# Kernel tuning notes

Measured on AMD Instinct MI355X. Metric: run time of the kernel, lower is better.

The kernel has to match this reference:

```python
import jax, jax.numpy as jnp
import numpy as np

P0 = 2   # tublet_size
P = 16   # patch_size
FC = 2   # flow channels (map_x, map_y)


def patchify(x, p0, p1, p2):
    # x: (B, C, T, H, W) -> (B, (T/p0)(H/p1)(W/p2), p0*p1*p2*C)
    B, C, T, H, W = x.shape
    x = x.reshape(B, C, T // p0, p0, H // p1, p1, W // p2, p2)
    x = x.transpose(0, 2, 4, 6, 3, 5, 7, 1)  # b t h w p0 p1 p2 c
    return x.reshape(B, (T // p0) * (H // p1) * (W // p2), p0 * p1 * p2 * C)


def unpatchify(x, p0, p1, p2, C, T, H, W):
    # x: (B, N, p0*p1*p2*C) -> (B, C, T, H, W)
    B = x.shape[0]
    x = x.reshape(B, T // p0, H // p1, W // p2, p0, p1, p2, C)
    x = x.transpose(0, 7, 1, 4, 2, 5, 3, 6)  # b c t p0 h p1 w p2
    return x.reshape(B, C, T, H, W)


def bilinear_warp(imgs, mx, my):
    # imgs: (B, C, T, H, W); mx, my: (B, T, H, W) absolute sample coords.
    # Equivalent of cv2.remap INTER_LINEAR with constant (zero) border.
    B, C, T, H, W = imgs.shape
    x0 = jnp.floor(mx)
    y0 = jnp.floor(my)
    wx = (mx - x0).reshape(B, 1, T, H * W)
    wy = (my - y0).reshape(B, 1, T, H * W)
    x0i = x0.astype(jnp.int32)
    y0i = y0.astype(jnp.int32)
    imgs_flat = imgs.reshape(B, C, T, H * W)

    def gather(yi, xi):
        yc = jnp.clip(yi, 0, H - 1)
        xc = jnp.clip(xi, 0, W - 1)
        idx = (yc * W + xc).reshape(B, 1, T, H * W)
        v = jnp.take_along_axis(imgs_flat, jnp.broadcast_to(idx, (B, C, T, H * W)), axis=-1)
        valid = ((yi >= 0) & (yi <= H - 1) & (xi >= 0) & (xi <= W - 1)).reshape(B, 1, T, H * W)
        return v * valid.astype(v.dtype)

    v00 = gather(y0i, x0i)
    v01 = gather(y0i, x0i + 1)
    v10 = gather(y0i + 1, x0i)
    v11 = gather(y0i + 1, x0i + 1)
    out = (v00 * (1 - wx) * (1 - wy) + v01 * wx * (1 - wy)
           + v10 * (1 - wx) * wy + v11 * wx * wy)
    return out.reshape(B, C, T, H, W)


def setup_inputs() -> dict:
    key = jax.random.key(0)
    k1, k2, k3 = jax.random.split(key, 3)
    B, C, T, H, W = 8, 3, 16, 224, 224
    N = (T // P0) * (H // P) * (W // P)         # 1568 tokens
    D = P0 * P * P * FC                         # 1024 per-token flow dim
    output = jax.random.normal(k1, (B, N, D), dtype=jnp.float32)
    raw_target = jax.random.normal(k2, (B, C, T, H, W), dtype=jnp.float32)
    mask = jax.random.randint(k3, (B, N), 0, 2) > 0
    return {"output": output, "raw_target": raw_target, "mask": mask}


def reference(output, raw_target, mask):
    B, C, T, H, W = raw_target.shape
    # tokens -> dense flow field (B, 2, T, H, W)
    flows = unpatchify(output, P0, P, P, FC, T, H, W)
    gx = jnp.arange(W, dtype=flows.dtype)               # (W,)
    gy = jnp.arange(H, dtype=flows.dtype)[:, None]      # (H, 1)
    mx = flows[:, 0] + gx                                # (B, T, H, W)
    my = flows[:, 1] + gy
    recons = bilinear_warp(raw_target, mx, my)           # (B, C, T, H, W)
    rec_p = patchify(recons, P0, P, P)                   # (B, N, p0*p1*p2*C)
    tgt_p = patchify(raw_target, P0, P, P)
    m = mask.astype(rec_p.dtype)[..., None]              # (B, N, 1)
    diff2 = (rec_p - tgt_p) ** 2 * m
    denom = jnp.maximum(m.sum(), 1.0) * rec_p.shape[-1]
    return diff2.sum() / denom
```

## Files before the change

kernel.cpp:

```cpp
#include <hip/hip_runtime.h>

#define Bd 8
#define Cd 3
#define Td 16
#define Hd 224
#define Wd 224
#define Nd 1568
#define Dd 1024
#define HWd (Hd*Wd)
#define MASK_N (Bd*Nd)
#define PATCH_ELEMS 1536.0

__global__ void flow_mse_tok(const float* __restrict__ outp,
                             const float* __restrict__ raw,
                             const int* __restrict__ mask,
                             float* __restrict__ partial) {
    const int tk = blockIdx.x;
    const int tid = threadIdx.x;

    if (mask[tk] == 0) {
        if (tid == 0) partial[tk] = 0.f;
        return;
    }

    const int b = tk / Nd;
    const int n = tk - b * Nd;
    const int t2  = n / 196;
    const int rem = n - t2 * 196;
    const int ph  = rem / 14;
    const int pw  = rem - ph * 14;

    const int i1 = tid >> 4;
    const int i2 = tid & 15;
    const int h = (ph << 4) + i1;
    const int w = (pw << 4) + i2;

    const float* fptr = outp + (size_t)tk * Dd;

    float acc = 0.f;
    #pragma unroll
    for (int i0 = 0; i0 < 2; ++i0) {
        const int t = (t2 << 1) + i0;
        float2 f = *(const float2*)(fptr + (((i0 << 8) + tid) << 1));
        float mx = f.x + (float)w;
        float my = f.y + (float)h;

        float x0 = floorf(mx), y0 = floorf(my);
        float wx = mx - x0,    wy = my - y0;
        int x0i = (int)x0, y0i = (int)y0;
        int x1i = x0i + 1, y1i = y0i + 1;

        bool vx0 = (x0i >= 0) && (x0i < Wd);
        bool vx1 = (x1i >= 0) && (x1i < Wd);
        bool vy0 = (y0i >= 0) && (y0i < Hd);
        bool vy1 = (y1i >= 0) && (y1i < Hd);

        int xc0 = min(max(x0i, 0), Wd - 1);
        int xc1 = min(max(x1i, 0), Wd - 1);
        int yc0 = min(max(y0i, 0), Hd - 1);
        int yc1 = min(max(y1i, 0), Hd - 1);

        float w00 = (1.f - wx) * (1.f - wy) * ((vx0 && vy0) ? 1.f : 0.f);
        float w01 = wx         * (1.f - wy) * ((vx1 && vy0) ? 1.f : 0.f);
        float w10 = (1.f - wx) * wy         * ((vx0 && vy1) ? 1.f : 0.f);
        float w11 = wx         * wy         * ((vx1 && vy1) ? 1.f : 0.f);

        int i00 = yc0 * Wd + xc0;
        int i01 = yc0 * Wd + xc1;
        int i10 = yc1 * Wd + xc0;
        int i11 = yc1 * Wd + xc1;
        int itg = h * Wd + w;

        #pragma unroll
        for (int c = 0; c < Cd; ++c) {
            const float* img = raw + (size_t)(((b * Cd + c) * Td + t)) * HWd;
            float v00 = img[i00];
            float v01 = img[i01];
            float v10 = img[i10];
            float v11 = img[i11];
            float rec = v00 * w00 + v01 * w01 + v10 * w10 + v11 * w11;
            float tgt = img[itg];
            float d = rec - tgt;
            acc += d * d;
        }
    }

    for (int off = 32; off > 0; off >>= 1) acc += __shfl_down(acc, off, 64);
    __shared__ float sdata[4];
    int lane = tid & 63, wid = tid >> 6;
    if (lane == 0) sdata[wid] = acc;
    __syncthreads();
    if (tid == 0)
        partial[tk] = sdata[0] + sdata[1] + sdata[2] + sdata[3];
}

__global__ void finalize_kernel(const float* __restrict__ partial,
                                const int* __restrict__ mask,
                                float* __restrict__ out) {
    double s = 0.0;
    for (int i = threadIdx.x; i < MASK_N; i += blockDim.x)
        s += (double)partial[i];
    int cnt = 0;
    for (int i = threadIdx.x; i < MASK_N; i += blockDim.x)
        cnt += (mask[i] != 0) ? 1 : 0;

    for (int off = 32; off > 0; off >>= 1) {
        s   += __shfl_down(s, off, 64);
        cnt += __shfl_down(cnt, off, 64);
    }
    __shared__ double sdat[4];
    __shared__ int    cdat[4];
    int lane = threadIdx.x & 63, wid = threadIdx.x >> 6;
    if (lane == 0) { sdat[wid] = s; cdat[wid] = cnt; }
    __syncthreads();
    if (threadIdx.x == 0) {
        double st = sdat[0] + sdat[1] + sdat[2] + sdat[3];
        int ct = cdat[0] + cdat[1] + cdat[2] + cdat[3];
        double denom = (double)(ct > 0 ? ct : 1) * PATCH_ELEMS;
        out[0] = (float)(st / denom);
    }
}

extern "C" void kernel_launch(void* const* d_in, const int* in_sizes, int n_in,
                              void* d_out, int out_size, void* d_ws, size_t ws_size,
                              hipStream_t stream) {
    const float* outp = (const float*)d_in[0];
    const float* raw  = (const float*)d_in[1];
    const int*   mask = (const int*)d_in[2];
    float* out = (float*)d_out;

    float* partial = (float*)d_ws;

    flow_mse_tok<<<MASK_N, 256, 0, stream>>>(outp, raw, mask, partial);
    finalize_kernel<<<1, 256, 0, stream>>>(partial, mask, out);
}
```

Measured before the change: 184.6 us.

## Stage 32x32 image window per token in LDS for bilinear gathers

Each unmasked token block now loads a 32x32 window of the source image around its 16x16 patch into shared memory, covering all 3 channels and 2 frames. The four bilinear taps and the target pixel are read from LDS when they fall inside the window, with a fallback to global gathers otherwise. This replaces scattered global gathers with coalesced window loads and cheap LDS reads. Because the flows are standard normal, most taps should land inside the window. The cost is a 30KB LDS footprint per block, which limits occupancy, plus an extra barrier. The finalize loops are also merged into one.

```diff
diff --git a/kernel.cpp b/kernel.cpp
--- a/kernel.cpp
+++ b/kernel.cpp
@@ -10,6 +10,10 @@
 #define HWd (Hd*Wd)
 #define MASK_N (Bd*Nd)
 #define PATCH_ELEMS 1536.0
+
+#define WIN 32
+#define PITCH 40
+#define PLANE (WIN*PITCH)
 
 __global__ void flow_mse_tok(const float* __restrict__ outp,
                              const float* __restrict__ raw,
@@ -30,10 +34,36 @@
     const int ph  = rem / 14;
     const int pw  = rem - ph * 14;
 
+    const int WX = min(max(pw * 16 - 8, 0), Wd - WIN);
+    const int WY = min(max(ph * 16 - 8, 0), Hd - WIN);
+
+    __shared__ float lds[6 * PLANE];
+
+    {
+        const int r  = tid >> 4;
+        const int cc = (tid & 15) << 1;
+        #pragma unroll
+        for (int p = 0; p < 6; ++p) {
+            const int c  = p >> 1;
+            const int i0 = p & 1;
+            const int t  = (t2 << 1) + i0;
+            const float* img = raw + (size_t)(((b * Cd + c) * Td + t)) * HWd;
+            float2 a = *(const float2*)(img + (WY + r)      * Wd + WX + cc);
+            float2 d = *(const float2*)(img + (WY + r + 16) * Wd + WX + cc);
+            float* pl = lds + p * PLANE;
+            pl[r * PITCH + cc]            = a.x;
+            pl[r * PITCH + cc + 1]        = a.y;
+            pl[(r + 16) * PITCH + cc]     = d.x;
+            pl[(r + 16) * PITCH + cc + 1] = d.y;
+        }
+    }
+    __syncthreads();
+
     const int i1 = tid >> 4;
     const int i2 = tid & 15;
     const int h = (ph << 4) + i1;
     const int w = (pw << 4) + i2;
+    const int tIdx = (h - WY) * PITCH + (w - WX);
 
     const float* fptr = outp + (size_t)tk * Dd;
 
@@ -65,23 +95,37 @@
         float w10 = (1.f - wx) * wy         * ((vx0 && vy1) ? 1.f : 0.f);
         float w11 = wx         * wy         * ((vx1 && vy1) ? 1.f : 0.f);
 
-        int i00 = yc0 * Wd + xc0;
-        int i01 = yc0 * Wd + xc1;
-        int i10 = yc1 * Wd + xc0;
-        int i11 = yc1 * Wd + xc1;
-        int itg = h * Wd + w;
+        const int lx0 = xc0 - WX, lx1 = xc1 - WX;
+        const int ly0 = yc0 - WY, ly1 = yc1 - WY;
+        const bool ok = (lx0 >= 0) & (lx1 < WIN) & (ly0 >= 0) & (ly1 < WIN);
 
-        #pragma unroll
-        for (int c = 0; c < Cd; ++c) {
-            const float* img = raw + (size_t)(((b * Cd + c) * Td + t)) * HWd;
-            float v00 = img[i00];
-            float v01 = img[i01];
-            float v10 = img[i10];
-            float v11 = img[i11];
-            float rec = v00 * w00 + v01 * w01 + v10 * w10 + v11 * w11;
-            float tgt = img[itg];
-            float d = rec - tgt;
-            acc += d * d;
+        if (ok) {
+            const int b00 = ly0 * PITCH + lx0;
+            const int b01 = ly0 * PITCH + lx1;
+            const int b10 = ly1 * PITCH + lx0;
+            const int b11 = ly1 * PITCH + lx1;
+            #pragma unroll
+            for (int c = 0; c < Cd; ++c) {
+                const float* pl = lds + ((c << 1) | i0) * PLANE;
+                float rec = pl[b00] * w00 + pl[b01] * w01
+                          + pl[b10] * w10 + pl[b11] * w11;
+                float d = rec - pl[tIdx];
+                acc += d * d;
+            }
+        } else {
+            const int i00 = yc0 * Wd + xc0;
+            const int i01 = yc0 * Wd + xc1;
+            const int i10 = yc1 * Wd + xc0;
+            const int i11 = yc1 * Wd + xc1;
+            #pragma unroll
+            for (int c = 0; c < Cd; ++c) {
+                const float* img = raw + (size_t)(((b * Cd + c) * Td + t)) * HWd;
+                float rec = img[i00] * w00 + img[i01] * w01
+                          + img[i10] * w10 + img[i11] * w11;
+                const float* pl = lds + ((c << 1) | i0) * PLANE;
+                float d = rec - pl[tIdx];
+                acc += d * d;
+            }
         }
     }
 
@@ -98,12 +142,11 @@
                                 const int* __restrict__ mask,
                                 float* __restrict__ out) {
     double s = 0.0;
-    for (int i = threadIdx.x; i < MASK_N; i += blockDim.x)
-        s += (double)partial[i];
     int cnt = 0;
-    for (int i = threadIdx.x; i < MASK_N; i += blockDim.x)
+    for (int i = threadIdx.x; i < MASK_N; i += blockDim.x) {
+        s   += (double)partial[i];
         cnt += (mask[i] != 0) ? 1 : 0;
-
+    }
     for (int off = 32; off > 0; off >>= 1) {
         s   += __shfl_down(s, off, 64);
         cnt += __shfl_down(cnt, off, 64);
```

After: 171.3 us. 7.2% less time.

## Compact masked tokens into list and process with persistent grid-stride kernel

Applied to the files above, without the earlier changes.

Adds a single-block compaction kernel that builds a list of active token indices and their count with a ballot-based prefix scan. The main kernel becomes a persistent 1024-block grid-stride loop over only active (token, pixel) work items, two per iteration, so about half the blocks no longer launch only to exit. Finalize now reduces 1024 partials and reads the count instead of rescanning the mask. This adds a serial one-block compaction launch and an extra indirection through the list.

```diff
diff --git a/kernel.cpp b/kernel.cpp
--- a/kernel.cpp
+++ b/kernel.cpp
@@ -10,113 +10,145 @@
 #define HWd (Hd*Wd)
 #define MASK_N (Bd*Nd)
 #define PATCH_ELEMS 1536.0
+#define GRID_MAIN 1024
+#define BLK 256
+#define STRIDE (GRID_MAIN*BLK)
 
-__global__ void flow_mse_tok(const float* __restrict__ outp,
-                             const float* __restrict__ raw,
-                             const int* __restrict__ mask,
-                             float* __restrict__ partial) {
-    const int tk = blockIdx.x;
-    const int tid = threadIdx.x;
+__device__ __forceinline__ float body(int g,
+                                      const float* __restrict__ outp,
+                                      const float* __restrict__ raw,
+                                      const int* __restrict__ list) {
+    const int slot = g >> 9;
+    const int s    = g & 511;
+    const int tk   = list[slot];
 
-    if (mask[tk] == 0) {
-        if (tid == 0) partial[tk] = 0.f;
-        return;
-    }
-
-    const int b = tk / Nd;
-    const int n = tk - b * Nd;
+    const int b   = tk / Nd;
+    const int n   = tk - b * Nd;
     const int t2  = n / 196;
     const int rem = n - t2 * 196;
     const int ph  = rem / 14;
     const int pw  = rem - ph * 14;
 
-    const int i1 = tid >> 4;
-    const int i2 = tid & 15;
-    const int h = (ph << 4) + i1;
-    const int w = (pw << 4) + i2;
+    const int i0  = s >> 8;
+    const int pix = s & 255;
+    const int h = (ph << 4) + (pix >> 4);
+    const int w = (pw << 4) + (pix & 15);
+    const int t = (t2 << 1) + i0;
 
-    const float* fptr = outp + (size_t)tk * Dd;
+    float2 f = *(const float2*)(outp + ((size_t)tk << 10) + (s << 1));
+    float mx = f.x + (float)w;
+    float my = f.y + (float)h;
+
+    float x0 = floorf(mx), y0 = floorf(my);
+    float wx = mx - x0,    wy = my - y0;
+    int x0i = (int)x0, y0i = (int)y0;
+    int x1i = x0i + 1, y1i = y0i + 1;
+
+    bool vx0 = (x0i >= 0) && (x0i < Wd);
+    bool vx1 = (x1i >= 0) && (x1i < Wd);
+    bool vy0 = (y0i >= 0) && (y0i < Hd);
+    bool vy1 = (y1i >= 0) && (y1i < Hd);
+
+    int xc0 = min(max(x0i, 0), Wd - 1);
+    int xc1 = min(max(x1i, 0), Wd - 1);
+    int yc0 = min(max(y0i, 0), Hd - 1);
+    int yc1 = min(max(y1i, 0), Hd - 1);
+
+    float w00 = (1.f - wx) * (1.f - wy) * ((vx0 && vy0) ? 1.f : 0.f);
+    float w01 = wx         * (1.f - wy) * ((vx1 && vy0) ? 1.f : 0.f);
+    float w10 = (1.f - wx) * wy         * ((vx0 && vy1) ? 1.f : 0.f);
+    float w11 = wx         * wy         * ((vx1 && vy1) ? 1.f : 0.f);
+
+    const int i00 = yc0 * Wd + xc0;
+    const int i01 = yc0 * Wd + xc1;
+    const int i10 = yc1 * Wd + xc0;
+    const int i11 = yc1 * Wd + xc1;
+    const int itg = h * Wd + w;
+
+    const float* img0 = raw + (size_t)(b * 48 + t) * HWd;
+    float acc = 0.f;
+    #pragma unroll
+    for (int c = 0; c < Cd; ++c) {
+        const float* img = img0 + c * (16 * HWd);
+        float v00 = img[i00];
+        float v01 = img[i01];
+        float v10 = img[i10];
+        float v11 = img[i11];
+        float tgt = img[itg];
+        float rec = v00 * w00 + v01 * w01 + v10 * w10 + v11 * w11;
+        float d = rec - tgt;
+        acc += d * d;
+    }
+    return acc;
+}
+
+__global__ void compact_kernel(const int* __restrict__ mask,
+                               int* __restrict__ list,
+                               unsigned int* __restrict__ cnt) {
+    const int tid = threadIdx.x;
+    __shared__ unsigned wt[16];
+    unsigned base = 0;
+    for (int i0 = 0; i0 < MASK_N; i0 += 1024) {
+        int i = i0 + tid;
+        bool m = (i < MASK_N) && (mask[i] != 0);
+        unsigned long long bal = __ballot(m);
+        int lane = tid & 63, wid = tid >> 6;
+        unsigned pre  = (unsigned)__popcll(bal & ((1ull << lane) - 1ull));
+        unsigned wtot = (unsigned)__popcll(bal);
+        if (lane == 0) wt[wid] = wtot;
+        __syncthreads();
+        unsigned wbase = base;
+        for (int k = 0; k < wid; ++k) wbase += wt[k];
+        if (m) list[wbase + pre] = i;
+        unsigned tot = 0;
+        #pragma unroll
+        for (int k = 0; k < 16; ++k) tot += wt[k];
+        base += tot;
+        __syncthreads();
+    }
+    if (tid == 0) *cnt = base;
+}
+
+__global__ void flow_mse_gather(const float* __restrict__ outp,
+                                const float* __restrict__ raw,
+                                const int* __restrict__ list,
+                                const unsigned int* __restrict__ cntp,
+                                float* __restrict__ partial) {
+    const int tid = threadIdx.x;
+    const int total = (int)(*cntp) << 9;
 
     float acc = 0.f;
-    #pragma unroll
-    for (int i0 = 0; i0 < 2; ++i0) {
-        const int t = (t2 << 1) + i0;
-        float2 f = *(const float2*)(fptr + (((i0 << 8) + tid) << 1));
-        float mx = f.x + (float)w;
-        float my = f.y + (float)h;
-
-        float x0 = floorf(mx), y0 = floorf(my);
-        float wx = mx - x0,    wy = my - y0;
-        int x0i = (int)x0, y0i = (int)y0;
-        int x1i = x0i + 1, y1i = y0i + 1;
-
-        bool vx0 = (x0i >= 0) && (x0i < Wd);
-        bool vx1 = (x1i >= 0) && (x1i < Wd);
-        bool vy0 = (y0i >= 0) && (y0i < Hd);
-        bool vy1 = (y1i >= 0) && (y1i < Hd);
-
-        int xc0 = min(max(x0i, 0), Wd - 1);
-        int xc1 = min(max(x1i, 0), Wd - 1);
-        int yc0 = min(max(y0i, 0), Hd - 1);
-        int yc1 = min(max(y1i, 0), Hd - 1);
-
-        float w00 = (1.f - wx) * (1.f - wy) * ((vx0 && vy0) ? 1.f : 0.f);
-        float w01 = wx         * (1.f - wy) * ((vx1 && vy0) ? 1.f : 0.f);
-        float w10 = (1.f - wx) * wy         * ((vx0 && vy1) ? 1.f : 0.f);
-        float w11 = wx         * wy         * ((vx1 && vy1) ? 1.f : 0.f);
-
-        int i00 = yc0 * Wd + xc0;
-        int i01 = yc0 * Wd + xc1;
-        int i10 = yc1 * Wd + xc0;
-        int i11 = yc1 * Wd + xc1;
-        int itg = h * Wd + w;
-
-        #pragma unroll
-        for (int c = 0; c < Cd; ++c) {
-            const float* img = raw + (size_t)(((b * Cd + c) * Td + t)) * HWd;
-            float v00 = img[i00];
-            float v01 = img[i01];
-            float v10 = img[i10];
-            float v11 = img[i11];
-            float rec = v00 * w00 + v01 * w01 + v10 * w10 + v11 * w11;
-            float tgt = img[itg];
-            float d = rec - tgt;
-            acc += d * d;
-        }
+    for (int g = blockIdx.x * BLK + tid; g < total; g += 2 * STRIDE) {
+        acc += body(g, outp, raw, list);
+        int g2 = g + STRIDE;
+        float a2 = body(min(g2, total - 1), outp, raw, list);
+        acc += (g2 < total) ? a2 : 0.f;
     }
 
     for (int off = 32; off > 0; off >>= 1) acc += __shfl_down(acc, off, 64);
     __shared__ float sdata[4];
-    int lane = tid & 63, wid = tid >> 6;
-    if (lane == 0) sdata[wid] = acc;
+    if ((tid & 63) == 0) sdata[tid >> 6] = acc;
     __syncthreads();
     if (tid == 0)
-        partial[tk] = sdata[0] + sdata[1] + sdata[2] + sdata[3];
+        partial[blockIdx.x] = sdata[0] + sdata[1] + sdata[2] + sdata[3];
 }
 
 __global__ void finalize_kernel(const float* __restrict__ partial,
-                                const int* __restrict__ mask,
+                                const unsigned int* __restrict__ cntp,
                                 float* __restrict__ out) {
     double s = 0.0;
-    for (int i = threadIdx.x; i < MASK_N; i += blockDim.x)
+    for (int i = threadIdx.x; i < GRID_MAIN; i += blockDim.x)
         s += (double)partial[i];
-    int cnt = 0;
-    for (int i = threadIdx.x; i < MASK_N; i += blockDim.x)
-        cnt += (mask[i] != 0) ? 1 : 0;
-
-    for (int off = 32; off > 0; off >>= 1) {
-        s   += __shfl_down(s, off, 64);
-        cnt += __shfl_down(cnt, off, 64);
-    }
+    for (int off = 32; off > 0; off >>= 1)
+        s += __shfl_down(s, off, 64);
     __shared__ double sdat[4];
-    __shared__ int    cdat[4];
     int lane = threadIdx.x & 63, wid = threadIdx.x >> 6;
-    if (lane == 0) { sdat[wid] = s; cdat[wid] = cnt; }
+    if (lane == 0) sdat[wid] = s;
     __syncthreads();
     if (threadIdx.x == 0) {
         double st = sdat[0] + sdat[1] + sdat[2] + sdat[3];
-        int ct = cdat[0] + cdat[1] + cdat[2] + cdat[3];
-        double denom = (double)(ct > 0 ? ct : 1) * PATCH_ELEMS;
+        unsigned ct = *cntp;
+        double denom = (double)(ct > 0u ? ct : 1u) * PATCH_ELEMS;
         out[0] = (float)(st / denom);
     }
 }
@@ -129,8 +161,11 @@
     const int*   mask = (const int*)d_in[2];
     float* out = (float*)d_out;
 
-    float* partial = (float*)d_ws;
+    unsigned int* cnt = (unsigned int*)d_ws;
+    float* partial = (float*)((char*)d_ws + 16);
+    int*   list    = (int*)((char*)d_ws + 16 + GRID_MAIN * 4);
 
-    flow_mse_tok<<<MASK_N, 256, 0, stream>>>(outp, raw, mask, partial);
-    finalize_kernel<<<1, 256, 0, stream>>>(partial, mask, out);
+    compact_kernel<<<1, 1024, 0, stream>>>(mask, list, cnt);
+    flow_mse_gather<<<GRID_MAIN, BLK, 0, stream>>>(outp, raw, list, cnt, partial);
+    finalize_kernel<<<1, 256, 0, stream>>>(partial, cnt, out);
 }
```

Measured after the change: 178.6 us. -3.3%, faster.
